# Optimization experiments

Measured on AMD Instinct MI355X. Metric: run time of the kernel, lower is better.

## Reference

```python
import jax, jax.numpy as jnp
import numpy as np

B, C_IN, C_OUT, H, K = 64, 64, 128, 1855, 6


def setup_inputs() -> dict:
    key = jax.random.key(0)
    k1, k2, k3, k4 = jax.random.split(key, 4)
    x = jax.random.normal(k1, (B, C_IN, H), dtype=jnp.float32)
    # neighbor table [H, K]; valid indices first, -1 padding at the end
    neighbors = jax.random.randint(k2, (H, K), 0, H)
    n_boundary = H // 10
    neighbors = neighbors.at[:n_boundary, K - 2:].set(-1)
    weight_center = jax.random.normal(k3, (C_OUT, C_IN), dtype=jnp.float32) / np.sqrt(C_IN).astype(np.float32)
    weight_neighbors = jax.random.normal(k4, (C_OUT, C_IN, K), dtype=jnp.float32) / np.sqrt(C_IN * K).astype(np.float32)
    bias = jnp.zeros((C_OUT,), dtype=jnp.float32)
    return {
        "x": x,
        "neighbors": neighbors,
        "weight_center": weight_center,
        "weight_neighbors": weight_neighbors,
        "bias": bias,
    }


def reference(x, neighbors, weight_center, weight_neighbors, bias):
    # x: [B, C_in, H]; neighbors: [H, K] with -1 = invalid (valid-first ordering)
    mask = neighbors >= 0                               # [H, K]
    idx = jnp.where(mask, neighbors, 0)                 # safe gather indices
    gathered = x[:, :, idx] * mask.astype(x.dtype)[None, None, :, :]  # [B, C_in, H, K]
    center = jnp.einsum('bch,oc->boh', x, weight_center)              # [B, C_out, H]
    neigh = jnp.einsum('bchk,ock->boh', gathered, weight_neighbors)   # [B, C_out, H]
    counts = (1 + mask.sum(axis=-1)).astype(x.dtype)                  # [H]
    return (center + neigh) / counts[None, None, :] + bias[None, :, None]
```

## Files before the change

kernel.cpp:

```cpp
#include <hip/hip_runtime.h>
#include <stdint.h>

typedef __bf16 bf16x8 __attribute__((ext_vector_type(8)));
typedef float floatx4 __attribute__((ext_vector_type(4)));
typedef unsigned short u16;
typedef unsigned int u32;

#define CIN   64
#define COUT  128
#define H_    1855
#define KNB   6
#define KTOT  448
#define NSTEPS 14
#define RS    456

static __device__ inline u16 f32_to_bf16(float f) {
    u32 u = __float_as_uint(f);
    u32 r = (u + 0x7FFFu + ((u >> 16) & 1u)) >> 16;
    return (u16)r;
}

__global__ __launch_bounds__(256) void k_transpose(const float* __restrict__ x,
                                                   u16* __restrict__ xt3) {
    __shared__ u16 tile[64][65];
    int h0  = blockIdx.x * 64;
    int bc0 = blockIdx.y * 64;
    int lane = threadIdx.x & 63;
    int rowq = threadIdx.x >> 6;
    int h = h0 + lane;
    bool hv = h < H_;
#pragma unroll
    for (int i = 0; i < 16; ++i) {
        int row = i * 4 + rowq;
        u16 v = 0;
        if (hv) v = f32_to_bf16(x[(size_t)(bc0 + row) * H_ + h]);
        tile[row][lane] = v;
    }
    __syncthreads();
#pragma unroll
    for (int i = 0; i < 16; ++i) {
        int hr = i * 4 + rowq;
        int hh = h0 + hr;
        if (hh < H_) xt3[(size_t)hh * 4096 + bc0 + lane] = tile[lane][hr];
    }
}

__global__ __launch_bounds__(256) void k_pack(const float* __restrict__ wc,
                                              const float* __restrict__ wn,
                                              const int* __restrict__ nbr,
                                              u16* __restrict__ wp,
                                              float* __restrict__ cInvG) {
    int tg = blockIdx.x * 256 + threadIdx.x;
    if (tg < H_) {
        int cnt = 1;
#pragma unroll
        for (int j = 0; j < KNB; ++j) cnt += (nbr[tg * KNB + j] >= 0) ? 1 : 0;
        cInvG[tg] = 1.0f / (float)cnt;
    }
    if (tg >= COUT * KTOT) return;
    int o = tg / KTOT;
    int rem = tg - o * KTOT;
    int s = rem >> 6, c = rem & 63;
    float v = (s == 0) ? wc[o * CIN + c]
                       : wn[(o * CIN + c) * KNB + (s - 1)];
    wp[tg] = f32_to_bf16(v);
}

__global__ __launch_bounds__(256, 2) void k_main(const u16* __restrict__ xt3,
                                                 const u16* __restrict__ wp,
                                                 const int* __restrict__ nbr,
                                                 const float* __restrict__ bias,
                                                 const float* __restrict__ cInvG,
                                                 float* __restrict__ out) {
    __shared__ __align__(16) u16 X[29248];

    int tid  = threadIdx.x;
    int g    = blockIdx.x;
    int boct = g & 7;
    int T    = g >> 3;
    int b0   = boct * 8;

    int lane = tid & 63;
    int wave = tid >> 6;
    int col  = lane & 15;
    int quad = lane >> 4;
    int m0w  = wave * 32;
    int bl   = lane >> 3;
    int chunk = lane & 7;

    bf16x8 afrag[2][NSTEPS];
#pragma unroll
    for (int mt = 0; mt < 2; ++mt) {
        int o = m0w + mt * 16 + col;
#pragma unroll
        for (int kk = 0; kk < NSTEPS; ++kk)
            afrag[mt][kk] = *(const bf16x8*)(wp + o * KTOT + kk * 32 + quad * 8);
    }
    float biasv[2][4];
#pragma unroll
    for (int mt = 0; mt < 2; ++mt)
#pragma unroll
        for (int r = 0; r < 4; ++r)
            biasv[mt][r] = bias[m0w + mt * 16 + quad * 4 + r];

#pragma unroll
    for (int tt = 0; tt < 2; ++tt) {
        int t = T * 2 + tt;
        int h0 = t * 8;
        __syncthreads();

#pragma unroll
        for (int i = 0; i < 14; ++i) {
            int hl = wave * 2 + (i < 7 ? 0 : 1);
            int s  = (i < 7) ? i : (i - 7);
            int h  = h0 + hl;
            int src = -1;
            if (h < H_) src = (s == 0) ? h : nbr[h * KNB + (s - 1)];
            uint4 v = make_uint4(0u, 0u, 0u, 0u);
            if (src >= 0)
                v = *(const uint4*)(xt3 + (size_t)src * 4096 + (b0 + bl) * 64 + chunk * 8);
            int n = bl * 8 + hl;
            *(uint4*)(X + n * RS + bl * 8 + s * 64 + chunk * 8) = v;
        }
        __syncthreads();

        floatx4 acc[2][4];
#pragma unroll
        for (int mt = 0; mt < 2; ++mt)
#pragma unroll
            for (int nt = 0; nt < 4; ++nt)
                acc[mt][nt] = (floatx4){0.0f, 0.0f, 0.0f, 0.0f};

        int rb[4];
#pragma unroll
        for (int nt = 0; nt < 4; ++nt) {
            int n = nt * 16 + col;
            rb[nt] = n * RS + (n >> 3) * 8 + quad * 8;
        }

#pragma unroll
        for (int kk = 0; kk < NSTEPS; ++kk) {
#pragma unroll
            for (int nt = 0; nt < 4; ++nt) {
                bf16x8 bfr = *(const bf16x8*)(X + rb[nt] + kk * 32);
                acc[0][nt] = __builtin_amdgcn_mfma_f32_16x16x32_bf16(
                    afrag[0][kk], bfr, acc[0][nt], 0, 0, 0);
                acc[1][nt] = __builtin_amdgcn_mfma_f32_16x16x32_bf16(
                    afrag[1][kk], bfr, acc[1][nt], 0, 0, 0);
            }
        }

        int hh = h0 + (col & 7);
        float ic = cInvG[hh < H_ ? hh : 0];
        bool hv = hh < H_;
#pragma unroll
        for (int nt = 0; nt < 4; ++nt) {
            int n = nt * 16 + col;
            size_t rowbase = ((size_t)(b0 + (n >> 3)) * COUT) * H_ + hh;
#pragma unroll
            for (int mt = 0; mt < 2; ++mt)
#pragma unroll
                for (int r = 0; r < 4; ++r) {
                    int o = m0w + mt * 16 + quad * 4 + r;
                    if (hv)
                        out[rowbase + (size_t)o * H_] =
                            acc[mt][nt][r] * ic + biasv[mt][r];
                }
        }
    }
}

extern "C" void kernel_launch(void* const* d_in, const int* in_sizes, int n_in,
                              void* d_out, int out_size, void* d_ws, size_t ws_size,
                              hipStream_t stream) {
    const float* x    = (const float*)d_in[0];
    const int*   nbr  = (const int*)d_in[1];
    const float* wc   = (const float*)d_in[2];
    const float* wn   = (const float*)d_in[3];
    const float* bias = (const float*)d_in[4];

    u16*   xt3   = (u16*)d_ws;
    u16*   wp    = (u16*)((char*)d_ws + (size_t)H_ * 4096 * 2);
    float* cInvG = (float*)((char*)d_ws + (size_t)H_ * 4096 * 2 + (size_t)COUT * KTOT * 2);

    k_pack<<<dim3((COUT * KTOT) / 256), dim3(256), 0, stream>>>(wc, wn, nbr, wp, cInvG);
    k_transpose<<<dim3(29, 64), dim3(256), 0, stream>>>(x, xt3);
    k_main<<<dim3(928), dim3(256), 0, stream>>>(xt3, wp, nbr, bias, cInvG, (float*)d_out);
}
```

Baseline: 155.6 us.

## Remap tiles to 2 batches x 32 hexes and stage output through LDS

Each block's tile changes from 8 batches x 8 hexes to 2 batches x 32 hexes, and the gather indexing is adjusted to match. Results are written to shared memory first and then stored so that 32 lanes write contiguous h positions per output row. Previously each store segment covered only 8 contiguous floats. The weight fragments are also pinned in registers with an empty asm constraint. The cost is smaller contiguous gather reads per neighbor row, plus an extra barrier and an LDS round trip in the epilogue.

```diff
diff --git a/kernel.cpp b/kernel.cpp
--- a/kernel.cpp
+++ b/kernel.cpp
@@ -3,6 +3,7 @@
 
 typedef __bf16 bf16x8 __attribute__((ext_vector_type(8)));
 typedef float floatx4 __attribute__((ext_vector_type(4)));
+typedef unsigned int u32x4 __attribute__((ext_vector_type(4)));
 typedef unsigned short u16;
 typedef unsigned int u32;
 
@@ -13,6 +14,8 @@
 #define KTOT  448
 #define NSTEPS 14
 #define RS    456
+
+#define PIN4(v) asm volatile("" : "+v"(v))
 
 static __device__ inline u16 f32_to_bf16(float f) {
     u32 u = __float_as_uint(f);
@@ -76,26 +79,32 @@
 
     int tid  = threadIdx.x;
     int g    = blockIdx.x;
-    int boct = g & 7;
-    int T    = g >> 3;
-    int b0   = boct * 8;
+    int bp   = g & 31;
+    int T    = g >> 5;
+    int b0   = bp * 2;
 
     int lane = tid & 63;
     int wave = tid >> 6;
     int col  = lane & 15;
     int quad = lane >> 4;
     int m0w  = wave * 32;
-    int bl   = lane >> 3;
+    int blg  = (lane >> 3) & 1;
     int chunk = lane & 7;
 
-    bf16x8 afrag[2][NSTEPS];
+    u32x4 afrag[2][NSTEPS];
 #pragma unroll
     for (int mt = 0; mt < 2; ++mt) {
         int o = m0w + mt * 16 + col;
 #pragma unroll
         for (int kk = 0; kk < NSTEPS; ++kk)
-            afrag[mt][kk] = *(const bf16x8*)(wp + o * KTOT + kk * 32 + quad * 8);
-    }
+            afrag[mt][kk] = *(const u32x4*)(wp + o * KTOT + kk * 32 + quad * 8);
+    }
+#pragma unroll
+    for (int mt = 0; mt < 2; ++mt)
+#pragma unroll
+        for (int kk = 0; kk < NSTEPS; ++kk)
+            PIN4(afrag[mt][kk]);
+
     float biasv[2][4];
 #pragma unroll
     for (int mt = 0; mt < 2; ++mt)
@@ -106,23 +115,27 @@
 #pragma unroll
     for (int tt = 0; tt < 2; ++tt) {
         int t = T * 2 + tt;
-        int h0 = t * 8;
+        int h0 = t * 32;
         __syncthreads();
 
 #pragma unroll
         for (int i = 0; i < 14; ++i) {
-            int hl = wave * 2 + (i < 7 ? 0 : 1);
+            int hl = wave * 8 + (i < 7 ? 0 : 4) + quad;
             int s  = (i < 7) ? i : (i - 7);
             int h  = h0 + hl;
             int src = -1;
             if (h < H_) src = (s == 0) ? h : nbr[h * KNB + (s - 1)];
-            uint4 v = make_uint4(0u, 0u, 0u, 0u);
+            u32x4 v = (u32x4){0u, 0u, 0u, 0u};
             if (src >= 0)
-                v = *(const uint4*)(xt3 + (size_t)src * 4096 + (b0 + bl) * 64 + chunk * 8);
-            int n = bl * 8 + hl;
-            *(uint4*)(X + n * RS + bl * 8 + s * 64 + chunk * 8) = v;
+                v = *(const u32x4*)(xt3 + (size_t)src * 4096 + (b0 + blg) * 64 + chunk * 8);
+            int n = blg * 32 + hl;
+            *(u32x4*)(X + n * RS + (n >> 3) * 8 + s * 64 + chunk * 8) = v;
         }
         __syncthreads();
+
+        int hA = h0 + col, hB = h0 + 16 + col;
+        float icA = cInvG[hA < H_ ? hA : 0];
+        float icB = cInvG[hB < H_ ? hB : 0];
 
         floatx4 acc[2][4];
 #pragma unroll
@@ -140,32 +153,42 @@
 
 #pragma unroll
         for (int kk = 0; kk < NSTEPS; ++kk) {
+            bf16x8 a0 = __builtin_bit_cast(bf16x8, afrag[0][kk]);
+            bf16x8 a1 = __builtin_bit_cast(bf16x8, afrag[1][kk]);
 #pragma unroll
             for (int nt = 0; nt < 4; ++nt) {
                 bf16x8 bfr = *(const bf16x8*)(X + rb[nt] + kk * 32);
                 acc[0][nt] = __builtin_amdgcn_mfma_f32_16x16x32_bf16(
-                    afrag[0][kk], bfr, acc[0][nt], 0, 0, 0);
+                    a0, bfr, acc[0][nt], 0, 0, 0);
                 acc[1][nt] = __builtin_amdgcn_mfma_f32_16x16x32_bf16(
-                    afrag[1][kk], bfr, acc[1][nt], 0, 0, 0);
+                    a1, bfr, acc[1][nt], 0, 0, 0);
             }
         }
 
-        int hh = h0 + (col & 7);
-        float ic = cInvG[hh < H_ ? hh : 0];
-        bool hv = hh < H_;
-#pragma unroll
-        for (int nt = 0; nt < 4; ++nt) {
-            int n = nt * 16 + col;
-            size_t rowbase = ((size_t)(b0 + (n >> 3)) * COUT) * H_ + hh;
-#pragma unroll
-            for (int mt = 0; mt < 2; ++mt)
+        __syncthreads();
+
+        float* stage = (float*)X;
+#pragma unroll
+        for (int mt = 0; mt < 2; ++mt)
+#pragma unroll
+            for (int nt = 0; nt < 4; ++nt) {
+                float ic = (nt & 1) ? icB : icA;
+                int n = nt * 16 + col;
 #pragma unroll
                 for (int r = 0; r < 4; ++r) {
                     int o = m0w + mt * 16 + quad * 4 + r;
-                    if (hv)
-                        out[rowbase + (size_t)o * H_] =
-                            acc[mt][nt][r] * ic + biasv[mt][r];
+                    stage[o * 66 + n] = acc[mt][nt][r] * ic + biasv[mt][r];
                 }
+            }
+
+        int hl2 = lane & 31, bl2 = lane >> 5;
+        int hh = h0 + hl2;
+        bool hv = hh < H_;
+#pragma unroll
+        for (int rr = 0; rr < 32; ++rr) {
+            int o = m0w + rr;
+            if (hv)
+                out[((size_t)(b0 + bl2) * COUT + o) * H_ + hh] = stage[o * 66 + lane];
         }
     }
 }
```

Result: no change. 153.2 us (-1.5%).

## Drop LDS staging in main kernel; load B fragments directly from global

Applied to the files above, without the earlier changes.

The main GEMM kernel no longer stages gathered neighbor rows in shared memory with barriers. Each wave now reads its bf16 B fragments straight from the transposed input through per-lane neighbor base pointers, and invalid neighbors point at a zeroed page. The grid is re-split into 512 blocks that partition work across batch pairs, output-channel quarters and strided h-tiles, with weights pinned in registers. This removes LDS traffic and syncs, but each wave computes a smaller 32x16 tile and issues more scattered global loads, so weight reuse per gathered row is lower.

```diff
diff --git a/kernel.cpp b/kernel.cpp
--- a/kernel.cpp
+++ b/kernel.cpp
@@ -3,6 +3,7 @@
 
 typedef __bf16 bf16x8 __attribute__((ext_vector_type(8)));
 typedef float floatx4 __attribute__((ext_vector_type(4)));
+typedef unsigned int u32x4 __attribute__((ext_vector_type(4)));
 typedef unsigned short u16;
 typedef unsigned int u32;
 
@@ -12,7 +13,13 @@
 #define KNB   6
 #define KTOT  448
 #define NSTEPS 14
-#define RS    456
+#define NT8   232
+
+#define WP_OFF   ((size_t)H_ * 4096 * 2)
+#define CINV_OFF (WP_OFF + (size_t)COUT * KTOT * 2)
+#define ZERO_OFF (CINV_OFF + 7424)
+
+#define PIN4(v) asm volatile("" : "+v"(v))
 
 static __device__ inline u16 f32_to_bf16(float f) {
     u32 u = __float_as_uint(f);
@@ -49,8 +56,10 @@
                                               const float* __restrict__ wn,
                                               const int* __restrict__ nbr,
                                               u16* __restrict__ wp,
-                                              float* __restrict__ cInvG) {
+                                              float* __restrict__ cInvG,
+                                              u32* __restrict__ zeroPg) {
     int tg = blockIdx.x * 256 + threadIdx.x;
+    if (tg < 32) zeroPg[tg] = 0u;
     if (tg < H_) {
         int cnt = 1;
 #pragma unroll
@@ -71,101 +80,82 @@
                                                  const int* __restrict__ nbr,
                                                  const float* __restrict__ bias,
                                                  const float* __restrict__ cInvG,
+                                                 const u16* __restrict__ zeroPg,
                                                  float* __restrict__ out) {
-    __shared__ __align__(16) u16 X[29248];
-
     int tid  = threadIdx.x;
     int g    = blockIdx.x;
-    int boct = g & 7;
-    int T    = g >> 3;
-    int b0   = boct * 8;
-
+    int wv   = tid >> 6;
     int lane = tid & 63;
-    int wave = tid >> 6;
     int col  = lane & 15;
     int quad = lane >> 4;
-    int m0w  = wave * 32;
-    int bl   = lane >> 3;
-    int chunk = lane & 7;
 
-    bf16x8 afrag[2][NSTEPS];
+    int bpLo = g & 7;
+    int bpHi = (g >> 3) & 3;
+    int mq   = (g >> 5) & 3;
+    int hq   = g >> 7;
+    int bp   = bpHi * 8 + bpLo;
+    int b0   = bp * 2;
+    int m0   = mq * 32;
+
+    int b_l  = col >> 3;
+    int h_l  = col & 7;
+    size_t bcol = (size_t)(b0 + b_l) * 64;
+
+    u32x4 afrag[2][NSTEPS];
 #pragma unroll
     for (int mt = 0; mt < 2; ++mt) {
-        int o = m0w + mt * 16 + col;
+        int o = m0 + mt * 16 + col;
 #pragma unroll
         for (int kk = 0; kk < NSTEPS; ++kk)
-            afrag[mt][kk] = *(const bf16x8*)(wp + o * KTOT + kk * 32 + quad * 8);
+            afrag[mt][kk] = *(const u32x4*)(wp + o * KTOT + kk * 32 + quad * 8);
     }
+#pragma unroll
+    for (int mt = 0; mt < 2; ++mt)
+#pragma unroll
+        for (int kk = 0; kk < NSTEPS; ++kk)
+            PIN4(afrag[mt][kk]);
+
     float biasv[2][4];
 #pragma unroll
     for (int mt = 0; mt < 2; ++mt)
 #pragma unroll
         for (int r = 0; r < 4; ++r)
-            biasv[mt][r] = bias[m0w + mt * 16 + quad * 4 + r];
+            biasv[mt][r] = bias[m0 + mt * 16 + quad * 4 + r];
 
+    for (int t = hq * 4 + wv; t < NT8; t += 16) {
+        int h  = t * 8 + h_l;
+        int hcl = h < H_ ? h : 0;
+        bool hv = h < H_;
+
+        const u16* base[7];
+        base[0] = xt3 + (size_t)hcl * 4096 + bcol;
 #pragma unroll
-    for (int tt = 0; tt < 2; ++tt) {
-        int t = T * 2 + tt;
-        int h0 = t * 8;
-        __syncthreads();
+        for (int s = 1; s < 7; ++s) {
+            int nv = nbr[hcl * KNB + (s - 1)];
+            base[s] = (nv >= 0) ? (xt3 + (size_t)nv * 4096 + bcol) : zeroPg;
+        }
 
-#pragma unroll
-        for (int i = 0; i < 14; ++i) {
-            int hl = wave * 2 + (i < 7 ? 0 : 1);
-            int s  = (i < 7) ? i : (i - 7);
-            int h  = h0 + hl;
-            int src = -1;
-            if (h < H_) src = (s == 0) ? h : nbr[h * KNB + (s - 1)];
-            uint4 v = make_uint4(0u, 0u, 0u, 0u);
-            if (src >= 0)
-                v = *(const uint4*)(xt3 + (size_t)src * 4096 + (b0 + bl) * 64 + chunk * 8);
-            int n = bl * 8 + hl;
-            *(uint4*)(X + n * RS + bl * 8 + s * 64 + chunk * 8) = v;
-        }
-        __syncthreads();
-
-        floatx4 acc[2][4];
-#pragma unroll
-        for (int mt = 0; mt < 2; ++mt)
-#pragma unroll
-            for (int nt = 0; nt < 4; ++nt)
-                acc[mt][nt] = (floatx4){0.0f, 0.0f, 0.0f, 0.0f};
-
-        int rb[4];
-#pragma unroll
-        for (int nt = 0; nt < 4; ++nt) {
-            int n = nt * 16 + col;
-            rb[nt] = n * RS + (n >> 3) * 8 + quad * 8;
-        }
+        floatx4 acc0 = (floatx4){0.f, 0.f, 0.f, 0.f};
+        floatx4 acc1 = (floatx4){0.f, 0.f, 0.f, 0.f};
 
 #pragma unroll
         for (int kk = 0; kk < NSTEPS; ++kk) {
-#pragma unroll
-            for (int nt = 0; nt < 4; ++nt) {
-                bf16x8 bfr = *(const bf16x8*)(X + rb[nt] + kk * 32);
-                acc[0][nt] = __builtin_amdgcn_mfma_f32_16x16x32_bf16(
-                    afrag[0][kk], bfr, acc[0][nt], 0, 0, 0);
-                acc[1][nt] = __builtin_amdgcn_mfma_f32_16x16x32_bf16(
-                    afrag[1][kk], bfr, acc[1][nt], 0, 0, 0);
-            }
+            bf16x8 bf = *(const bf16x8*)(base[kk >> 1] + (kk & 1) * 32 + quad * 8);
+            acc0 = __builtin_amdgcn_mfma_f32_16x16x32_bf16(
+                __builtin_bit_cast(bf16x8, afrag[0][kk]), bf, acc0, 0, 0, 0);
+            acc1 = __builtin_amdgcn_mfma_f32_16x16x32_bf16(
+                __builtin_bit_cast(bf16x8, afrag[1][kk]), bf, acc1, 0, 0, 0);
         }
 
-        int hh = h0 + (col & 7);
-        float ic = cInvG[hh < H_ ? hh : 0];
-        bool hv = hh < H_;
+        float ic = cInvG[hcl];
+        size_t obase = ((size_t)(b0 + b_l) * COUT) * H_ + h;
 #pragma unroll
-        for (int nt = 0; nt < 4; ++nt) {
-            int n = nt * 16 + col;
-            size_t rowbase = ((size_t)(b0 + (n >> 3)) * COUT) * H_ + hh;
-#pragma unroll
-            for (int mt = 0; mt < 2; ++mt)
-#pragma unroll
-                for (int r = 0; r < 4; ++r) {
-                    int o = m0w + mt * 16 + quad * 4 + r;
-                    if (hv)
-                        out[rowbase + (size_t)o * H_] =
-                            acc[mt][nt][r] * ic + biasv[mt][r];
-                }
+        for (int r = 0; r < 4; ++r) {
+            int o0 = m0 + quad * 4 + r;
+            if (hv) {
+                out[obase + (size_t)o0 * H_]        = acc0[r] * ic + biasv[0][r];
+                out[obase + (size_t)(o0 + 16) * H_] = acc1[r] * ic + biasv[1][r];
+            }
         }
     }
 }
@@ -179,11 +169,14 @@
     const float* wn   = (const float*)d_in[3];
     const float* bias = (const float*)d_in[4];
 
-    u16*   xt3   = (u16*)d_ws;
-    u16*   wp    = (u16*)((char*)d_ws + (size_t)H_ * 4096 * 2);
-    float* cInvG = (float*)((char*)d_ws + (size_t)H_ * 4096 * 2 + (size_t)COUT * KTOT * 2);
+    u16*   xt3    = (u16*)d_ws;
+    u16*   wp     = (u16*)((char*)d_ws + WP_OFF);
+    float* cInvG  = (float*)((char*)d_ws + CINV_OFF);
+    u32*   zeroPg = (u32*)((char*)d_ws + ZERO_OFF);
 
-    k_pack<<<dim3((COUT * KTOT) / 256), dim3(256), 0, stream>>>(wc, wn, nbr, wp, cInvG);
+    k_pack<<<dim3((COUT * KTOT + 255) / 256), dim3(256), 0, stream>>>(
+        wc, wn, nbr, wp, cInvG, zeroPg);
     k_transpose<<<dim3(29, 64), dim3(256), 0, stream>>>(x, xt3);
-    k_main<<<dim3(928), dim3(256), 0, stream>>>(xt3, wp, nbr, bias, cInvG, (float*)d_out);
+    k_main<<<dim3(512), dim3(256), 0, stream>>>(
+        xt3, wp, nbr, bias, cInvG, (const u16*)zeroPg, (float*)d_out);
 }
```

Result: slower. 160.1 us (+2.9%).
